# Performance work log

Measured on AMD Instinct MI355X. Metric: run time of the kernel, lower is better.

The kernel has to match this reference:

```python
import jax, jax.numpy as jnp
import numpy as np

H = 384          # hidden_dim == filter_size == n_chans
N_BINS = 256
PRED_GRAD = 0.1
LN_EPS = 1e-5


def _conv1d_same(x_bct, w_oik, b):
    k = w_oik.shape[-1]
    p = (k - 1) // 2
    y = jax.lax.conv_general_dilated(
        x_bct, w_oik, window_strides=(1,), padding=[(p, p)],
        dimension_numbers=("NCT", "OIT", "NCT"))
    return y + b[None, :, None]


def _ln_last(x, g, b):  # LayerNorm over last dim
    m = jnp.mean(x, axis=-1, keepdims=True)
    v = jnp.var(x, axis=-1, keepdims=True)
    return (x - m) * jax.lax.rsqrt(v + LN_EPS) * g + b


def _ln_chan(x_bct, g, b):  # LayerNorm over channel dim (dim=1)
    m = jnp.mean(x_bct, axis=1, keepdims=True)
    v = jnp.var(x_bct, axis=1, keepdims=True)
    return (x_bct - m) * jax.lax.rsqrt(v + LN_EPS) * g[None, :, None] + b[None, :, None]


def _sin_pos(x0, dim):
    # fairseq SinusoidalPositionalEmbedding, padding_idx=0, applied to xs[...,0]
    mask = (x0 != 0).astype(jnp.int32)
    pos = jnp.cumsum(mask, axis=1) * mask                        # [B,T]
    half = dim // 2
    inv = jnp.exp(jnp.arange(half, dtype=jnp.float32) * (-(np.log(10000.0) / (half - 1))))
    ang = pos[..., None].astype(jnp.float32) * inv               # [B,T,half]
    pe = jnp.concatenate([jnp.sin(ang), jnp.cos(ang)], axis=-1)  # [B,T,dim]
    return jnp.where(pos[..., None] == 0, 0.0, pe)


def _duration_predictor(x, src_mask, w1, b1, g1, be1, w2, b2, g2, be2, lw, lb):
    h = _conv1d_same(jnp.swapaxes(x, 1, 2), w1, b1)
    h = _ln_last(jax.nn.relu(jnp.swapaxes(h, 1, 2)), g1, be1)
    h = _conv1d_same(jnp.swapaxes(h, 1, 2), w2, b2)
    h = _ln_last(jax.nn.relu(jnp.swapaxes(h, 1, 2)), g2, be2)
    out = (h @ lw + lb)[..., 0]                                  # [B,T]
    return jnp.where(src_mask, 0.0, out)


def _variance_predictor(x, cw, cb, g, b, lw, lb, alpha):
    pos = alpha * _sin_pos(x[..., 0], x.shape[-1])
    h = jnp.swapaxes(x + pos, 1, 2)                              # [B,C,T]
    for i in range(cw.shape[0]):
        h = _ln_chan(jax.nn.relu(_conv1d_same(h, cw[i], cb[i])), g[i], b[i])
    return jnp.swapaxes(h, 1, 2) @ lw + lb                       # [B,T,odim]


def _length_regulate(x, dur_int, max_len):
    B, T, _ = x.shape
    cum = jnp.cumsum(dur_int, axis=1)                            # [B,T]
    frames = jnp.arange(max_len)
    idx = jax.vmap(lambda c: jnp.searchsorted(c, frames, side="right"))(cum)
    idx = jnp.clip(idx, 0, T - 1)                                # [B,max_len]
    out = jnp.take_along_axis(x, idx[..., None], axis=1)         # [B,max_len,H]
    total = cum[:, -1]
    valid = frames[None, :] < total[:, None]
    out = jnp.where(valid[..., None], out, 0.0)
    mel_len = jnp.minimum(total, max_len)
    return out, mel_len


def setup_inputs() -> dict:
    key = jax.random.key(0)
    ks = iter(jax.random.split(key, 40))
    B, T = 32, 1024
    rnd = lambda s: 0.02 * jax.random.normal(next(ks), s, dtype=jnp.float32)
    inp = {
        "x": jax.random.normal(next(ks), (B, T, H), dtype=jnp.float32),
        "src_lens": jax.random.randint(next(ks), (B,), 0, T),
        "src_mask": jnp.zeros((B, T), dtype=bool),
        "max_len": 4096,
        # duration predictor (kernel=3)
        "dp_w1": rnd((H, H, 3)), "dp_b1": jnp.zeros((H,)),
        "dp_ln1_g": jnp.ones((H,)), "dp_ln1_b": jnp.zeros((H,)),
        "dp_w2": rnd((H, H, 3)), "dp_b2": jnp.zeros((H,)),
        "dp_ln2_g": jnp.ones((H,)), "dp_ln2_b": jnp.zeros((H,)),
        "dp_lw": rnd((H, 1)), "dp_lb": jnp.full((1,), 1.5),  # bias -> avg dur ~3.5
        # pitch predictor: 5 layers, kernel=5, odim=1 (use_uv=False)
        "pp_cw": rnd((5, H, H, 5)), "pp_cb": jnp.zeros((5, H)),
        "pp_g": jnp.ones((5, H)), "pp_b": jnp.zeros((5, H)),
        "pp_lw": rnd((H, 1)), "pp_lb": jnp.zeros((1,)), "pp_alpha": jnp.ones((1,)),
        # energy predictor: 2 layers, kernel=5, odim=1
        "ep_cw": rnd((2, H, H, 5)), "ep_cb": jnp.zeros((2, H)),
        "ep_g": jnp.ones((2, H)), "ep_b": jnp.zeros((2, H)),
        "ep_lw": rnd((H, 1)), "ep_lb": jnp.zeros((1,)), "ep_alpha": jnp.ones((1,)),
        # bins (requires_grad=False buffers) + embedding tables
        "pitch_bins": jnp.linspace(-4.0, 4.0, N_BINS - 1),
        "energy_bins": jnp.linspace(-4.0, 4.0, N_BINS - 1),
        "pitch_table": rnd((N_BINS, H)),
        "energy_table": rnd((N_BINS, H)),
    }
    return inp


def reference(x, src_lens, src_mask, max_len,
              dp_w1, dp_b1, dp_ln1_g, dp_ln1_b, dp_w2, dp_b2, dp_ln2_g, dp_ln2_b, dp_lw, dp_lb,
              pp_cw, pp_cb, pp_g, pp_b, pp_lw, pp_lb, pp_alpha,
              ep_cw, ep_cb, ep_g, ep_b, ep_lw, ep_lb, ep_alpha,
              pitch_bins, energy_bins, pitch_table, energy_table):
    # duration (inference path: no targets, controls = 1.0)
    log_d = _duration_predictor(x, src_mask, dp_w1, dp_b1, dp_ln1_g, dp_ln1_b,
                                dp_w2, dp_b2, dp_ln2_g, dp_ln2_b, dp_lw, dp_lb)
    dur = jnp.clip(jnp.round(jnp.exp(log_d) - 1.0), 0.0, None)
    dur_int = dur.astype(jnp.int32)

    # straight-through-style grad scaling on predictor inputs
    xg = jax.lax.stop_gradient(x) + PRED_GRAD * (x - jax.lax.stop_gradient(x))

    # phoneme-level pitch (use_uv=False -> squeeze, bucketize)
    pitch_pred = _variance_predictor(xg, pp_cw, pp_cb, pp_g, pp_b, pp_lw, pp_lb, pp_alpha)[..., 0]
    pitch_idx = jnp.searchsorted(pitch_bins, pitch_pred, side="left")  # torch.bucketize(right=False)
    pitch_emb = pitch_table[pitch_idx]

    # phoneme-level energy
    energy_pred = _variance_predictor(xg, ep_cw, ep_cb, ep_g, ep_b, ep_lw, ep_lb, ep_alpha)[..., 0]
    energy_idx = jnp.searchsorted(energy_bins, energy_pred, side="left")
    energy_emb = energy_table[energy_idx]

    x_adapt = x + pitch_emb + energy_emb
    out, mel_len = _length_regulate(x_adapt, dur_int, int(max_len))
    return out, log_d, dur, pitch_pred, energy_pred, mel_len
```

## Files before the change

kernel.cpp:

```cpp
#include <hip/hip_runtime.h>
#include <cstdint>

#define HH 384
#define NBINS 256

typedef __attribute__((ext_vector_type(8))) short short8v;
typedef __attribute__((ext_vector_type(16))) float f32x16;
typedef __attribute__((ext_vector_type(4))) unsigned short ushort4v;

__device__ inline float4 ld4(const float* p){ return *(const float4*)p; }

__device__ inline unsigned short bf16_rne(float f){
  unsigned u = __float_as_uint(f);
  unsigned r = u + 0x7FFFu + ((u >> 16) & 1u);
  return (unsigned short)(r >> 16);
}
__device__ inline float bf16_to_f(unsigned short h){
  return __uint_as_float(((unsigned)h) << 16);
}

__global__ __launch_bounds__(1024) void pos_kernel(const float* __restrict__ x,
    int* __restrict__ pos, int T)
{
  __shared__ int s[1024];
  int b = blockIdx.x, tid = threadIdx.x;
  int m = 0;
  if (tid < T) m = (x[((size_t)b*T + tid)*HH] != 0.f) ? 1 : 0;
  s[tid] = m;
  __syncthreads();
  for (int off = 1; off < 1024; off <<= 1){
    int add = (tid >= off) ? s[tid-off] : 0;
    __syncthreads();
    s[tid] += add;
    __syncthreads();
  }
  if (tid < T) pos[(size_t)b*T + tid] = s[tid] * m;
}

__global__ __launch_bounds__(HH) void add_pe_kernel(const float* __restrict__ x,
    const int* __restrict__ pos, const float* __restrict__ alpha,
    float* __restrict__ out)
{
  int row = blockIdx.x; int i = threadIdx.x;
  int p = pos[row];
  float pe = 0.f;
  if (p != 0){
    int j = (i < HH/2) ? i : i - HH/2;
    float inv = expf((float)j * -0.04822167734018944f);
    float ang = (float)p * inv;
    pe = (i < HH/2) ? sinf(ang) : cosf(ang);
  }
  out[(size_t)row*HH + i] = x[(size_t)row*HH + i] + alpha[0]*pe;
}

template<int K>
__global__ __launch_bounds__(256) void wtrans_kernel(const float* __restrict__ w,
    unsigned short* __restrict__ dst, int nlayers)
{
  constexpr int SPL = (24*K + 2) * 6144;
  const int per = 384*384;
  int gid = blockIdx.x*256 + threadIdx.x;
  if (gid >= nlayers*per) return;
  int l = gid / per, rem = gid - l*per;
  int o = rem / 384, i = rem - (rem/384)*384;
  unsigned short* whi = dst + (size_t)l*2*SPL;
  unsigned short* wlo = whi + SPL;
  const float* wl = w + (size_t)l*384*384*K;
  int c = i >> 4, half = (i >> 3) & 1, jj = i & 7;
  #pragma unroll
  for (int k = 0; k < K; ++k){
    float v = wl[((size_t)o*384 + i)*K + k];
    unsigned short hi = bf16_rne(v);
    unsigned short lo = bf16_rne(v - bf16_to_f(hi));
    int s = k*24 + c;
    size_t d = ((size_t)(s*2 + half)*384 + o)*8 + jj;
    whi[d] = hi; wlo[d] = lo;
  }
}

template<int K>
__global__ __launch_bounds__(256) void conv_mfma_kernel(
    const float* __restrict__ in, const unsigned short* __restrict__ whi,
    const unsigned short* __restrict__ wlo, const float* __restrict__ bias,
    const float* __restrict__ g, const float* __restrict__ be,
    float* __restrict__ out, int T)
{
  constexpr int MT = 32;
  constexpr int P  = (K-1)/2;
  constexpr int RT = MT + K - 1;
  constexpr int RA = RT + 2;
  constexpr int NS = 24*K;
  constexpr int LDP = 392;
  __shared__ unsigned short xs_hi[RA*LDP];
  __shared__ unsigned short xs_lo[RA*LDP];
  __shared__ float ps[4][32], pq[4][32];

  int ntile = T / MT;
  int b  = blockIdx.x / ntile;
  int t0 = (blockIdx.x % ntile) * MT;
  int tid = threadIdx.x;
  const float* inb = in + (size_t)b*T*HH;

  {
    constexpr int TOT4 = RT*96;
    for (int e4 = tid; e4 < TOT4; e4 += 256){
      int r = e4 / 96, c4 = (e4 - r*96)*4;
      int t = t0 + r - P;
      float4 v = (t >= 0 && t < T) ? ld4(&inb[(size_t)t*HH + c4])
                                   : make_float4(0.f,0.f,0.f,0.f);
      float va[4] = {v.x, v.y, v.z, v.w};
      ushort4v h, l;
      #pragma unroll
      for (int q = 0; q < 4; ++q){
        unsigned short hq = bf16_rne(va[q]);
        h[q] = hq;
        l[q] = bf16_rne(va[q] - bf16_to_f(hq));
      }
      *(ushort4v*)&xs_hi[r*LDP + c4] = h;
      *(ushort4v*)&xs_lo[r*LDP + c4] = l;
    }
  }
  __syncthreads();

  int wv = tid >> 6, ln = tid & 63;
  int l31 = ln & 31, hl = ln >> 5;
  int o0 = wv * 96;

  const unsigned short* bhp = whi + ((size_t)hl*384 + o0 + l31)*8;
  const unsigned short* blp = wlo + ((size_t)hl*384 + o0 + l31)*8;
  int aoff = l31*LDP + hl*8;
  int cc = 0;

  f32x16 acc[3];
  #pragma unroll
  for (int nt = 0; nt < 3; ++nt){
    float bv = bias[o0 + nt*32 + l31];
    #pragma unroll
    for (int r = 0; r < 16; ++r) acc[nt][r] = bv;
  }

  short8v B0h[3], B0l[3], B1h[3], B1l[3], B2h[3], B2l[3];
  short8v A0h, A0l, A1h, A1l, A2h, A2l;

#define ADV do{ bhp += 6144; blp += 6144; aoff += 16;                        \
                if (++cc == 24){ cc = 0; aoff += LDP - 384; } }while(0)

  #pragma unroll
  for (int nt = 0; nt < 3; ++nt){
    B0h[nt] = *(const short8v*)(bhp + nt*256);
    B0l[nt] = *(const short8v*)(blp + nt*256);
  }
  A0h = *(const short8v*)&xs_hi[aoff];
  A0l = *(const short8v*)&xs_lo[aoff];
  ADV;
  #pragma unroll
  for (int nt = 0; nt < 3; ++nt){
    B1h[nt] = *(const short8v*)(bhp + nt*256);
    B1l[nt] = *(const short8v*)(blp + nt*256);
  }
  A1h = *(const short8v*)&xs_hi[aoff];
  A1l = *(const short8v*)&xs_lo[aoff];
  ADV;

#define PHASE(NBh,NBl,NAh,NAl,CBh,CBl,CAh,CAl) do{                           \
    _Pragma("unroll")                                                        \
    for (int nt = 0; nt < 3; ++nt){                                          \
      NBh[nt] = *(const short8v*)(bhp + nt*256);                             \
      NBl[nt] = *(const short8v*)(blp + nt*256);                             \
    }                                                                        \
    NAh = *(const short8v*)&xs_hi[aoff];                                     \
    NAl = *(const short8v*)&xs_lo[aoff];                                     \
    ADV;                                                                     \
    __builtin_amdgcn_sched_barrier(0);                                       \
    __builtin_amdgcn_s_setprio(1);                                           \
    _Pragma("unroll")                                                        \
    for (int nt = 0; nt < 3; ++nt)                                           \
      acc[nt] = __builtin_amdgcn_mfma_f32_32x32x16_bf16(CAh, CBh[nt], acc[nt], 0,0,0); \
    _Pragma("unroll")                                                        \
    for (int nt = 0; nt < 3; ++nt)                                           \
      acc[nt] = __builtin_amdgcn_mfma_f32_32x32x16_bf16(CAh, CBl[nt], acc[nt], 0,0,0); \
    _Pragma("unroll")                                                        \
    for (int nt = 0; nt < 3; ++nt)                                           \
      acc[nt] = __builtin_amdgcn_mfma_f32_32x32x16_bf16(CAl, CBh[nt], acc[nt], 0,0,0); \
    __builtin_amdgcn_s_setprio(0);                                           \
  } while(0)

  for (int s = 0; s < NS; s += 3){
    PHASE(B2h,B2l,A2h,A2l, B0h,B0l,A0h,A0l);
    PHASE(B0h,B0l,A0h,A0l, B1h,B1l,A1h,A1l);
    PHASE(B1h,B1l,A1h,A1l, B2h,B2l,A2h,A2l);
  }
#undef PHASE
#undef ADV

  float gv[3], bev[3];
  #pragma unroll
  for (int nt = 0; nt < 3; ++nt){
    gv[nt]  = g[o0 + nt*32 + l31];
    bev[nt] = be[o0 + nt*32 + l31];
  }

  #pragma unroll
  for (int r = 0; r < 16; ++r){
    float s1 = 0.f, s2 = 0.f;
    #pragma unroll
    for (int nt = 0; nt < 3; ++nt){
      float v = fmaxf(acc[nt][r], 0.f);
      acc[nt][r] = v;
      s1 += v; s2 += v*v;
    }
    s1 += __shfl_xor(s1, 1);  s2 += __shfl_xor(s2, 1);
    s1 += __shfl_xor(s1, 2);  s2 += __shfl_xor(s2, 2);
    s1 += __shfl_xor(s1, 4);  s2 += __shfl_xor(s2, 4);
    s1 += __shfl_xor(s1, 8);  s2 += __shfl_xor(s2, 8);
    s1 += __shfl_xor(s1, 16); s2 += __shfl_xor(s2, 16);
    if (l31 == 0){
      int t = (r&3) + 8*(r>>2) + 4*hl;
      ps[wv][t] = s1; pq[wv][t] = s2;
    }
  }
  __syncthreads();

  #pragma unroll
  for (int r = 0; r < 16; ++r){
    int t = (r&3) + 8*(r>>2) + 4*hl;
    float s1 = ps[0][t] + ps[1][t] + ps[2][t] + ps[3][t];
    float s2 = pq[0][t] + pq[1][t] + pq[2][t] + pq[3][t];
    float mn  = s1 * (1.f/HH);
    float var = fmaxf(s2 * (1.f/HH) - mn*mn, 0.f);
    float rr  = rsqrtf(var + 1e-5f);
    float* orow = out + ((size_t)b*T + t0 + t)*HH;
    #pragma unroll
    for (int nt = 0; nt < 3; ++nt)
      orow[o0 + nt*32 + l31] = (acc[nt][r] - mn)*rr*gv[nt] + bev[nt];
  }
}

__global__ __launch_bounds__(256) void proj_var_kernel(const float* __restrict__ h,
    const float* __restrict__ lw, const float* __restrict__ lb,
    const float* __restrict__ bins, float* __restrict__ pred,
    int* __restrict__ idx, int nrows)
{
  int lane = threadIdx.x & 63, wid = threadIdx.x >> 6;
  int wave = blockIdx.x*4 + wid, nw = gridDim.x*4;
  float lwr[6];
  #pragma unroll
  for (int j = 0; j < 6; ++j) lwr[j] = lw[lane + 64*j];
  float lbv = lb[0];
  for (int row = wave; row < nrows; row += nw){
    const float* hr = h + (size_t)row*HH;
    float s = 0.f;
    #pragma unroll
    for (int j = 0; j < 6; ++j) s = fmaf(hr[lane + 64*j], lwr[j], s);
    #pragma unroll
    for (int off = 32; off; off >>= 1) s += __shfl_xor(s, off);
    if (lane == 0){
      float v = s + lbv;
      pred[row] = v;
      int lo = 0, hi = NBINS - 1;
      while (lo < hi){ int mid = (lo + hi) >> 1; if (bins[mid] < v) lo = mid + 1; else hi = mid; }
      idx[row] = lo;
    }
  }
}

__global__ __launch_bounds__(256) void proj_dur_kernel(const float* __restrict__ h,
    const float* __restrict__ lw, const float* __restrict__ lb,
    const unsigned char* __restrict__ mask, float* __restrict__ logd,
    float* __restrict__ durf, int* __restrict__ duri, int nrows)
{
  int lane = threadIdx.x & 63, wid = threadIdx.x >> 6;
  int wave = blockIdx.x*4 + wid, nw = gridDim.x*4;
  float lwr[6];
  #pragma unroll
  for (int j = 0; j < 6; ++j) lwr[j] = lw[lane + 64*j];
  float lbv = lb[0];
  for (int row = wave; row < nrows; row += nw){
    const float* hr = h + (size_t)row*HH;
    float s = 0.f;
    #pragma unroll
    for (int j = 0; j < 6; ++j) s = fmaf(hr[lane + 64*j], lwr[j], s);
    #pragma unroll
    for (int off = 32; off; off >>= 1) s += __shfl_xor(s, off);
    if (lane == 0){
      float v = s + lbv;
      if (mask[row]) v = 0.f;
      logd[row] = v;
      float d = fmaxf(rintf(expf(v) - 1.f), 0.f);
      durf[row] = d;
      duri[row] = (int)d;
    }
  }
}

__global__ __launch_bounds__(1024) void cumsum_kernel(const int* __restrict__ duri,
    int* __restrict__ cum, float* __restrict__ mel, int T, int ML)
{
  __shared__ int s[1024];
  int b = blockIdx.x, tid = threadIdx.x;
  s[tid] = (tid < T) ? duri[(size_t)b*T + tid] : 0;
  __syncthreads();
  for (int off = 1; off < 1024; off <<= 1){
    int add = (tid >= off) ? s[tid-off] : 0;
    __syncthreads();
    s[tid] += add;
    __syncthreads();
  }
  if (tid < T) cum[(size_t)b*T + tid] = s[tid];
  if (tid == T-1) mel[b] = (float)min(s[tid], ML);
}

__global__ __launch_bounds__(256) void xadapt_kernel(const float* __restrict__ x,
    const int* __restrict__ ip, const int* __restrict__ ie,
    const float* __restrict__ pt, const float* __restrict__ et,
    float* __restrict__ xa, int nrows)
{
  int gid = blockIdx.x*256 + threadIdx.x;
  int n4 = nrows * (HH/4);
  if (gid >= n4) return;
  int row = gid / (HH/4);
  int c = gid - row*(HH/4);
  float4 xv = ((const float4*)x)[gid];
  const float4* pr = (const float4*)(pt + (size_t)ip[row]*HH);
  const float4* er = (const float4*)(et + (size_t)ie[row]*HH);
  float4 pv = pr[c], ev = er[c];
  ((float4*)xa)[gid] = make_float4(xv.x+pv.x+ev.x, xv.y+pv.y+ev.y,
                                   xv.z+pv.z+ev.z, xv.w+pv.w+ev.w);
}

__global__ __launch_bounds__(256) void lr_kernel(const float* __restrict__ xa,
    const int* __restrict__ cum, float* __restrict__ out, int T, int ML)
{
  constexpr int FR = 32;
  __shared__ int scum[1024];
  __shared__ int sidx[FR];
  __shared__ int svalid[FR];
  int b  = blockIdx.y;
  int f0 = blockIdx.x * FR;
  for (int i = threadIdx.x; i < T; i += 256) scum[i] = cum[(size_t)b*T + i];
  __syncthreads();
  int total = scum[T-1];
  if (threadIdx.x < FR){
    int f = f0 + threadIdx.x;
    int lo = 0, hi = T;
    while (lo < hi){ int mid = (lo + hi) >> 1; if (scum[mid] <= f) lo = mid + 1; else hi = mid; }
    sidx[threadIdx.x] = min(lo, T-1);
    svalid[threadIdx.x] = (f < total) ? 1 : 0;
  }
  __syncthreads();
  #pragma unroll
  for (int it = 0; it < FR*(HH/4)/256; ++it){
    int item = it*256 + threadIdx.x;
    int fl = item / (HH/4);
    int c  = item - fl*(HH/4);
    int f  = f0 + fl;
    if (f >= ML) continue;
    float4 v = make_float4(0.f,0.f,0.f,0.f);
    if (svalid[fl]) v = ((const float4*)(xa + ((size_t)b*T + sidx[fl])*HH))[c];
    ((float4*)(out + ((size_t)b*ML + f)*HH))[c] = v;
  }
}

extern "C" void kernel_launch(void* const* d_in, const int* in_sizes, int n_in,
                              void* d_out, int out_size, void* d_ws, size_t ws_size,
                              hipStream_t stream)
{
  const float* x        = (const float*)d_in[0];
  const unsigned char* src_mask = (const unsigned char*)d_in[2];
  const float* dp_w1 = (const float*)d_in[4];
  const float* dp_b1 = (const float*)d_in[5];
  const float* dp_g1 = (const float*)d_in[6];
  const float* dp_be1= (const float*)d_in[7];
  const float* dp_w2 = (const float*)d_in[8];
  const float* dp_b2 = (const float*)d_in[9];
  const float* dp_g2 = (const float*)d_in[10];
  const float* dp_be2= (const float*)d_in[11];
  const float* dp_lw = (const float*)d_in[12];
  const float* dp_lb = (const float*)d_in[13];
  const float* pp_cw = (const float*)d_in[14];
  const float* pp_cb = (const float*)d_in[15];
  const float* pp_g  = (const float*)d_in[16];
  const float* pp_b  = (const float*)d_in[17];
  const float* pp_lw = (const float*)d_in[18];
  const float* pp_lb = (const float*)d_in[19];
  const float* pp_alpha = (const float*)d_in[20];
  const float* ep_cw = (const float*)d_in[21];
  const float* ep_cb = (const float*)d_in[22];
  const float* ep_g  = (const float*)d_in[23];
  const float* ep_b  = (const float*)d_in[24];
  const float* ep_lw = (const float*)d_in[25];
  const float* ep_lb = (const float*)d_in[26];
  const float* ep_alpha = (const float*)d_in[27];
  const float* pbins = (const float*)d_in[28];
  const float* ebins = (const float*)d_in[29];
  const float* ptab  = (const float*)d_in[30];
  const float* etab  = (const float*)d_in[31];

  int B = in_sizes[1];
  int T = in_sizes[0] / (B*HH);
  int ML = (int)(((long long)out_size - B - 4LL*B*T) / ((long long)B*HH));
  size_t rows = (size_t)B*T;

  float* bufA = (float*)d_ws;
  float* bufB = bufA + rows*HH;
  int* pos    = (int*)(bufB + rows*HH);
  int* idx_p  = pos + rows;
  int* idx_e  = idx_p + rows;
  int* dur_i  = idx_e + rows;
  int* cum    = dur_i + rows;

  float* out0    = (float*)d_out;
  float* logd    = out0 + (size_t)B*ML*HH;
  float* durf    = logd + rows;
  float* pitchp  = durf + rows;
  float* energyp = pitchp + rows;
  float* mel     = energyp + rows;

  const size_t SPL5 = (size_t)(24*5 + 2)*6144;
  const size_t SPL3 = (size_t)(24*3 + 2)*6144;
  unsigned short* wsc    = (unsigned short*)d_out;
  unsigned short* pitchW = wsc;
  unsigned short* enerW  = pitchW + 5*2*SPL5;
  unsigned short* durW1  = enerW  + 2*2*SPL5;
  unsigned short* durW2  = durW1  + 2*SPL3;

  const int per = 384*384;
  wtrans_kernel<5><<<(5*per + 255)/256, 256, 0, stream>>>(pp_cw, pitchW, 5);
  wtrans_kernel<5><<<(2*per + 255)/256, 256, 0, stream>>>(ep_cw, enerW, 2);
  wtrans_kernel<3><<<(per + 255)/256, 256, 0, stream>>>(dp_w1, durW1, 1);
  wtrans_kernel<3><<<(per + 255)/256, 256, 0, stream>>>(dp_w2, durW2, 1);

  int conv_grid = B * (T / 32);

  pos_kernel<<<B, 1024, 0, stream>>>(x, pos, T);

  add_pe_kernel<<<(int)rows, HH, 0, stream>>>(x, pos, pp_alpha, bufA);
  {
    float* src = bufA; float* dst = bufB;
    for (int l = 0; l < 5; ++l){
      unsigned short* whi = pitchW + (size_t)l*2*SPL5;
      conv_mfma_kernel<5><<<conv_grid, 256, 0, stream>>>(src, whi, whi + SPL5,
          pp_cb + (size_t)l*HH, pp_g + (size_t)l*HH, pp_b + (size_t)l*HH, dst, T);
      float* t2 = dst; dst = src; src = t2;
    }
    proj_var_kernel<<<256, 256, 0, stream>>>(src, pp_lw, pp_lb, pbins,
                                             pitchp, idx_p, (int)rows);
  }

  add_pe_kernel<<<(int)rows, HH, 0, stream>>>(x, pos, ep_alpha, bufA);
  {
    float* src = bufA; float* dst = bufB;
    for (int l = 0; l < 2; ++l){
      unsigned short* whi = enerW + (size_t)l*2*SPL5;
      conv_mfma_kernel<5><<<conv_grid, 256, 0, stream>>>(src, whi, whi + SPL5,
          ep_cb + (size_t)l*HH, ep_g + (size_t)l*HH, ep_b + (size_t)l*HH, dst, T);
      float* t2 = dst; dst = src; src = t2;
    }
    proj_var_kernel<<<256, 256, 0, stream>>>(src, ep_lw, ep_lb, ebins,
                                             energyp, idx_e, (int)rows);
  }

  conv_mfma_kernel<3><<<conv_grid, 256, 0, stream>>>(x, durW1, durW1 + SPL3,
      dp_b1, dp_g1, dp_be1, bufB, T);
  conv_mfma_kernel<3><<<conv_grid, 256, 0, stream>>>(bufB, durW2, durW2 + SPL3,
      dp_b2, dp_g2, dp_be2, bufA, T);
  proj_dur_kernel<<<256, 256, 0, stream>>>(bufA, dp_lw, dp_lb, src_mask,
                                           logd, durf, dur_i, (int)rows);

  cumsum_kernel<<<B, 1024, 0, stream>>>(dur_i, cum, mel, T, ML);

  xadapt_kernel<<<(int)((rows*(HH/4) + 255)/256), 256, 0, stream>>>(
      x, idx_p, idx_e, ptab, etab, bufB, (int)rows);

  lr_kernel<<<dim3(ML/32, B), 256, 0, stream>>>(bufB, cum, out0, T, ML);
}
```

Baseline: 1.593 ms.

## Split conv input channels into two halves to shrink shared-memory tile

The conv MFMA kernel now stages the input tile in two 192-channel phases instead of all 384 channels at once, roughly halving the shared-memory footprint per block. The weight-transform kernel reorders the packed bf16 hi/lo weights so each channel half is contiguous. The intent is to fit more blocks per CU for better latency hiding. The cost is an extra barrier and reload per block, plus pipeline prologue overhead repeated for each phase.

```diff
diff --git a/kernel.cpp b/kernel.cpp
--- a/kernel.cpp
+++ b/kernel.cpp
@@ -66,13 +66,15 @@
   unsigned short* whi = dst + (size_t)l*2*SPL;
   unsigned short* wlo = whi + SPL;
   const float* wl = w + (size_t)l*384*384*K;
-  int c = i >> 4, half = (i >> 3) & 1, jj = i & 7;
+  int ph = (i >= 192) ? 1 : 0;
+  int iloc = i - 192*ph;
+  int c = iloc >> 4, half = (iloc >> 3) & 1, jj = iloc & 7;
   #pragma unroll
   for (int k = 0; k < K; ++k){
     float v = wl[((size_t)o*384 + i)*K + k];
     unsigned short hi = bf16_rne(v);
     unsigned short lo = bf16_rne(v - bf16_to_f(hi));
-    int s = k*24 + c;
+    int s = ph*12*K + k*12 + c;
     size_t d = ((size_t)(s*2 + half)*384 + o)*8 + jj;
     whi[d] = hi; wlo[d] = lo;
   }
@@ -85,14 +87,14 @@
     const float* __restrict__ g, const float* __restrict__ be,
     float* __restrict__ out, int T)
 {
-  constexpr int MT = 32;
-  constexpr int P  = (K-1)/2;
-  constexpr int RT = MT + K - 1;
-  constexpr int RA = RT + 2;
-  constexpr int NS = 24*K;
-  constexpr int LDP = 392;
-  __shared__ unsigned short xs_hi[RA*LDP];
-  __shared__ unsigned short xs_lo[RA*LDP];
+  constexpr int MT  = 32;
+  constexpr int P   = (K-1)/2;
+  constexpr int RT  = MT + K - 1;
+  constexpr int RA  = RT + 2;
+  constexpr int SPH = 12*K;
+  constexpr int LDPc = 200;
+  __shared__ unsigned short xs_hi[RA*LDPc];
+  __shared__ unsigned short xs_lo[RA*LDPc];
   __shared__ float ps[4][32], pq[4][32];
 
   int ntile = T / MT;
@@ -101,12 +103,25 @@
   int tid = threadIdx.x;
   const float* inb = in + (size_t)b*T*HH;
 
-  {
-    constexpr int TOT4 = RT*96;
-    for (int e4 = tid; e4 < TOT4; e4 += 256){
-      int r = e4 / 96, c4 = (e4 - r*96)*4;
+  int wv = tid >> 6, ln = tid & 63;
+  int l31 = ln & 31, hl = ln >> 5;
+  int o0 = wv * 96;
+
+  f32x16 acc[3];
+  #pragma unroll
+  for (int nt = 0; nt < 3; ++nt){
+    float bv = bias[o0 + nt*32 + l31];
+    #pragma unroll
+    for (int r = 0; r < 16; ++r) acc[nt][r] = bv;
+  }
+
+  for (int phse = 0; phse < 2; ++phse){
+    if (phse) __syncthreads();
+
+    for (int e4 = tid; e4 < RT*48; e4 += 256){
+      int r = e4 / 48, c4 = (e4 - r*48)*4;
       int t = t0 + r - P;
-      float4 v = (t >= 0 && t < T) ? ld4(&inb[(size_t)t*HH + c4])
+      float4 v = (t >= 0 && t < T) ? ld4(&inb[(size_t)t*HH + phse*192 + c4])
                                    : make_float4(0.f,0.f,0.f,0.f);
       float va[4] = {v.x, v.y, v.z, v.w};
       ushort4v h, l;
@@ -116,51 +131,40 @@
         h[q] = hq;
         l[q] = bf16_rne(va[q] - bf16_to_f(hq));
       }
-      *(ushort4v*)&xs_hi[r*LDP + c4] = h;
-      *(ushort4v*)&xs_lo[r*LDP + c4] = l;
-    }
-  }
-  __syncthreads();
-
-  int wv = tid >> 6, ln = tid & 63;
-  int l31 = ln & 31, hl = ln >> 5;
-  int o0 = wv * 96;
-
-  const unsigned short* bhp = whi + ((size_t)hl*384 + o0 + l31)*8;
-  const unsigned short* blp = wlo + ((size_t)hl*384 + o0 + l31)*8;
-  int aoff = l31*LDP + hl*8;
-  int cc = 0;
-
-  f32x16 acc[3];
-  #pragma unroll
-  for (int nt = 0; nt < 3; ++nt){
-    float bv = bias[o0 + nt*32 + l31];
-    #pragma unroll
-    for (int r = 0; r < 16; ++r) acc[nt][r] = bv;
-  }
-
-  short8v B0h[3], B0l[3], B1h[3], B1l[3], B2h[3], B2l[3];
-  short8v A0h, A0l, A1h, A1l, A2h, A2l;
+      *(ushort4v*)&xs_hi[r*LDPc + c4] = h;
+      *(ushort4v*)&xs_lo[r*LDPc + c4] = l;
+    }
+    __syncthreads();
+
+    const unsigned short* bhp = whi + (size_t)phse*SPH*6144
+                                    + ((size_t)hl*384 + o0 + l31)*8;
+    const unsigned short* blp = wlo + (size_t)phse*SPH*6144
+                                    + ((size_t)hl*384 + o0 + l31)*8;
+    int aoff = l31*LDPc + hl*8;
+    int cc = 0;
+
+    short8v B0h[3], B0l[3], B1h[3], B1l[3], B2h[3], B2l[3];
+    short8v A0h, A0l, A1h, A1l, A2h, A2l;
 
 #define ADV do{ bhp += 6144; blp += 6144; aoff += 16;                        \
-                if (++cc == 24){ cc = 0; aoff += LDP - 384; } }while(0)
-
-  #pragma unroll
-  for (int nt = 0; nt < 3; ++nt){
-    B0h[nt] = *(const short8v*)(bhp + nt*256);
-    B0l[nt] = *(const short8v*)(blp + nt*256);
-  }
-  A0h = *(const short8v*)&xs_hi[aoff];
-  A0l = *(const short8v*)&xs_lo[aoff];
-  ADV;
-  #pragma unroll
-  for (int nt = 0; nt < 3; ++nt){
-    B1h[nt] = *(const short8v*)(bhp + nt*256);
-    B1l[nt] = *(const short8v*)(blp + nt*256);
-  }
-  A1h = *(const short8v*)&xs_hi[aoff];
-  A1l = *(const short8v*)&xs_lo[aoff];
-  ADV;
+                if (++cc == 12){ cc = 0; aoff += LDPc - 192; } }while(0)
+
+    #pragma unroll
+    for (int nt = 0; nt < 3; ++nt){
+      B0h[nt] = *(const short8v*)(bhp + nt*256);
+      B0l[nt] = *(const short8v*)(blp + nt*256);
+    }
+    A0h = *(const short8v*)&xs_hi[aoff];
+    A0l = *(const short8v*)&xs_lo[aoff];
+    ADV;
+    #pragma unroll
+    for (int nt = 0; nt < 3; ++nt){
+      B1h[nt] = *(const short8v*)(bhp + nt*256);
+      B1l[nt] = *(const short8v*)(blp + nt*256);
+    }
+    A1h = *(const short8v*)&xs_hi[aoff];
+    A1l = *(const short8v*)&xs_lo[aoff];
+    ADV;
 
 #define PHASE(NBh,NBl,NAh,NAl,CBh,CBl,CAh,CAl) do{                           \
     _Pragma("unroll")                                                        \
@@ -185,13 +189,14 @@
     __builtin_amdgcn_s_setprio(0);                                           \
   } while(0)
 
-  for (int s = 0; s < NS; s += 3){
-    PHASE(B2h,B2l,A2h,A2l, B0h,B0l,A0h,A0l);
-    PHASE(B0h,B0l,A0h,A0l, B1h,B1l,A1h,A1l);
-    PHASE(B1h,B1l,A1h,A1l, B2h,B2l,A2h,A2l);
-  }
+    for (int s = 0; s < SPH; s += 3){
+      PHASE(B2h,B2l,A2h,A2l, B0h,B0l,A0h,A0l);
+      PHASE(B0h,B0l,A0h,A0l, B1h,B1l,A1h,A1l);
+      PHASE(B1h,B1l,A1h,A1l, B2h,B2l,A2h,A2l);
+    }
 #undef PHASE
 #undef ADV
+  }
 
   float gv[3], bev[3];
   #pragma unroll
```

After: 1.615 ms. About the same (+1.3%).
